# Kernel tuning notes

Measured on AMD Instinct MI355X. Metric: run time of the kernel, lower is better.

## Reference

```python
import jax, jax.numpy as jnp
import numpy as np

N = 4096          # number_of_node
DIN = 3           # dim_input (forced: fc1 expects N*dim_input == N*3 after last stage)
DOUT = 4          # dim_output
DACT = N          # dim_action defaults to number_of_node
B = 128


def setup_inputs() -> dict:
    key = jax.random.key(0)
    ks = jax.random.split(key, 12)
    X = jax.random.normal(ks[0], (B, N * DIN), dtype=jnp.float32)
    adj = jax.random.uniform(ks[1], (N, N), dtype=jnp.float32)
    def lin(kw, kb, fan_in, fan_out):
        bound = 1.0 / np.sqrt(fan_in)
        W = jax.random.uniform(kw, (fan_in, fan_out), minval=-bound, maxval=bound, dtype=jnp.float32)
        b = jax.random.uniform(kb, (fan_out,), minval=-bound, maxval=bound, dtype=jnp.float32)
        return W, b
    W1, b1 = lin(ks[2], ks[3], DIN, 4)
    W2, b2 = lin(ks[4], ks[5], 4, DOUT)
    W3, b3 = lin(ks[6], ks[7], DOUT, 3)
    Wfc, bfc = lin(ks[8], ks[9], N * DIN, 54)
    Wout, bout = lin(ks[10], ks[11], 54, DACT)
    return {"X": X, "adj": adj, "W1": W1, "b1": b1, "W2": W2, "b2": b2,
            "W3": W3, "b3": b3, "Wfc": Wfc, "bfc": bfc, "Wout": Wout, "bout": bout}


def reference(X, adj, W1, b1, W2, b2, W3, b3, Wfc, bfc, Wout, bout):
    # X: [B, N*DIN] -> [B, N, DIN]
    h = X.reshape(X.shape[0], N, DIN)
    # three (adj @ h) aggregations fused with tiny Linear + ReLU
    h = jax.nn.relu(jnp.einsum('nm,bmf->bnf', adj, h) @ W1 + b1)   # [B,N,4]
    h = jax.nn.relu(jnp.einsum('nm,bmf->bnf', adj, h) @ W2 + b2)   # [B,N,DOUT]
    h = jax.nn.relu(jnp.einsum('nm,bmf->bnf', adj, h) @ W3 + b3)   # [B,N,3]
    flat = h.reshape(h.shape[0], -1)                               # [B, N*3]
    hid = jax.nn.relu(flat @ Wfc + bfc)                            # [B, 54]
    q_value = hid @ Wout + bout                                    # [B, DACT]
    return q_value
```

## Files before the change

### kernel.cpp

```cpp
#include <hip/hip_runtime.h>


typedef __bf16 bf16x8 __attribute__((ext_vector_type(8)));
typedef float  f32x4  __attribute__((ext_vector_type(4)));

#define N_NODE 4096
#define BATCH  128

__device__ __forceinline__ void async_copy16(const void* gsrc, void* ldst) {
    __builtin_amdgcn_global_load_lds(
        (const __attribute__((address_space(1))) void*)gsrc,
        (__attribute__((address_space(3))) void*)ldst,
        16, 0, 0);
}

__global__ __launch_bounds__(256) void prep_k(const float* __restrict__ adj,
                                              __bf16* __restrict__ adjB,
                                              const float* __restrict__ X,
                                              const float* __restrict__ W1,
                                              __bf16* __restrict__ G0,
                                              float* __restrict__ hid_acc) {
    const int blk = blockIdx.x, tx = threadIdx.x;
    if (blk < 8192) {
        const size_t i = (size_t)blk * 256 + tx;
        const float4* a4 = (const float4*)adj;
        float4 u = a4[i * 2];
        float4 v = a4[i * 2 + 1];
        bf16x8 o = { (__bf16)u.x, (__bf16)u.y, (__bf16)u.z, (__bf16)u.w,
                     (__bf16)v.x, (__bf16)v.y, (__bf16)v.z, (__bf16)v.w };
        *(bf16x8*)(adjB + i * 8) = o;
    } else if (blk < 9216) {
        const int g = (blk - 8192) * 256 + tx;
        const int lp = g & 63, cbg = (g >> 6) & 31, kc = g >> 11;
        const int c = cbg * 16 + (lp & 15);
        const int b = c >> 2, f = c & 3;
        const float w0 = W1[0 * 4 + f], w1 = W1[1 * 4 + f], w2 = W1[2 * 4 + f];
        const int mb = kc * 32 + ((lp >> 4) & 3) * 8;
        const float* Xb = X + (size_t)b * 12288 + (size_t)mb * 3;
        bf16x8 o;
#pragma unroll
        for (int j = 0; j < 8; ++j) {
            const float v = Xb[j * 3 + 0] * w0 + Xb[j * 3 + 1] * w1 + Xb[j * 3 + 2] * w2;
            o[j] = (__bf16)v;
        }
        *(bf16x8*)(G0 + (size_t)g * 8) = o;
    } else {
        const int i = (blk - 9216) * 256 + tx;
        if (i < BATCH * 54) hid_acc[i] = 0.f;
    }
}

template <int MODE>
__global__ __launch_bounds__(256, 2) void gcn_k(const __bf16* __restrict__ A,
                                                const __bf16* __restrict__ Bp,
                                                const float* __restrict__ Wa,
                                                const float* __restrict__ ba,
                                                const float* __restrict__ Wb,
                                                __bf16* __restrict__ Op,
                                                float* __restrict__ H3out) {
    __shared__ __align__(16) unsigned char smem[65536];
    const int tx = threadIdx.x;
    const int wk = tx >> 6, lane = tx & 63;
    const int quad = lane >> 4, lr = lane & 15;

    const int l = blockIdx.x;
    const int xcd = l & 7, s = l >> 3;
    const int mi = xcd * 8 + (s & 7), ci = s >> 3;
    const int m0 = mi * 64, c0 = ci * 64;

    const __bf16* gA[4];
#pragma unroll
    for (int q = 0; q < 4; ++q) {
        const int c = q * 256 + tx;
        const int r = c >> 4, p = c & 15;
        const int lk = (p - r) & 15;
        gA[q] = A + (size_t)(m0 + r) * 4096 + lk * 8;
    }
    const __bf16* gB[4];
#pragma unroll
    for (int j = 0; j < 4; ++j)
        gB[j] = Bp + ((size_t)((wk * 32 + (ci * 4 + j)) * 64 + lane)) * 8;

    const int posw = ((wk * 4 + quad + lr) & 15) * 8;
    int foffA[4];
#pragma unroll
    for (int i = 0; i < 4; ++i) foffA[i] = (i * 16 + lr) * 128 + posw;

    f32x4 acc[4][4] = {};
    bf16x8 bv0[4], bv1[4], bv2[4], bv3[4];

#pragma unroll
    for (int q = 0; q < 4; ++q) async_copy16(gA[q], smem + q * 4096 + tx * 16);
#pragma unroll
    for (int j = 0; j < 4; ++j) bv0[j] = *(const bf16x8*)(gB[j]);
    asm volatile("" ::: "memory");
#pragma unroll
    for (int q = 0; q < 4; ++q) async_copy16(gA[q] + 128, smem + 16384 + q * 4096 + tx * 16);
#pragma unroll
    for (int j = 0; j < 4; ++j) bv1[j] = *(const bf16x8*)(gB[j] + 65536);
    asm volatile("" ::: "memory");
#pragma unroll
    for (int q = 0; q < 4; ++q) async_copy16(gA[q] + 256, smem + 32768 + q * 4096 + tx * 16);
#pragma unroll
    for (int j = 0; j < 4; ++j) bv2[j] = *(const bf16x8*)(gB[j] + 131072);
    asm volatile("" ::: "memory");

#define GCN_STEP(KT, P, WAIT, PF, CUR, NXT)                                    \
    {                                                                          \
        asm volatile(WAIT ::: "memory");                                       \
        __builtin_amdgcn_s_barrier();                                          \
        const __bf16* Ab = (const __bf16*)(smem + (P) * 16384);                \
        bf16x8 af[4];                                                          \
        _Pragma("unroll") for (int i = 0; i < 4; ++i)                          \
            af[i] = *(const bf16x8*)(Ab + foffA[i]);                           \
        if (PF) {                                                              \
            const int nt_ = (KT) + 3;                                          \
            unsigned char* bo_ = smem + (((P) + 3) & 3) * 16384;               \
            _Pragma("unroll") for (int q = 0; q < 4; ++q)                      \
                async_copy16(gA[q] + nt_ * 128, bo_ + q * 4096 + tx * 16);     \
            _Pragma("unroll") for (int j = 0; j < 4; ++j)                      \
                NXT[j] = *(const bf16x8*)(gB[j] + (size_t)nt_ * 65536);        \
        }                                                                      \
        __builtin_amdgcn_s_setprio(1);                                         \
        _Pragma("unroll") for (int i = 0; i < 4; ++i)                          \
            _Pragma("unroll") for (int j = 0; j < 4; ++j)                      \
                acc[i][j] = __builtin_amdgcn_mfma_f32_16x16x32_bf16(           \
                    af[i], CUR[j], acc[i][j], 0, 0, 0);                        \
        __builtin_amdgcn_s_setprio(0);                                         \
    }

    for (int kt = 0; kt < 28; kt += 4) {
        GCN_STEP(kt + 0, 0, "s_waitcnt vmcnt(16) lgkmcnt(0)", 1, bv0, bv3)
        GCN_STEP(kt + 1, 1, "s_waitcnt vmcnt(16) lgkmcnt(0)", 1, bv1, bv0)
        GCN_STEP(kt + 2, 2, "s_waitcnt vmcnt(16) lgkmcnt(0)", 1, bv2, bv1)
        GCN_STEP(kt + 3, 3, "s_waitcnt vmcnt(16) lgkmcnt(0)", 1, bv3, bv2)
    }
    GCN_STEP(28, 0, "s_waitcnt vmcnt(16) lgkmcnt(0)", 1, bv0, bv3)
    GCN_STEP(29, 1, "s_waitcnt vmcnt(16) lgkmcnt(0)", 0, bv1, bv0)
    GCN_STEP(30, 2, "s_waitcnt vmcnt(8) lgkmcnt(0)",  0, bv2, bv1)
    GCN_STEP(31, 3, "s_waitcnt vmcnt(0) lgkmcnt(0)",  0, bv3, bv2)
#undef GCN_STEP

    __syncthreads();
    float* part = (float*)smem;
    const int sb = (wk >> 1) * 4096;
    if (wk & 1) {
#pragma unroll
        for (int t = 0; t < 16; ++t)
            *(f32x4*)(part + sb + t * 256 + lane * 4) = acc[t >> 2][t & 3];
    }
    __syncthreads();
    if (!(wk & 1)) {
#pragma unroll
        for (int t = 0; t < 16; ++t)
            acc[t >> 2][t & 3] += *(const f32x4*)(part + sb + t * 256 + lane * 4);
    }
    __syncthreads();
    if (wk == 2) {
#pragma unroll
        for (int t = 0; t < 16; ++t)
            *(f32x4*)(part + t * 256 + lane * 4) = acc[t >> 2][t & 3];
    }
    __syncthreads();
    float* Ct = (float*)(smem + 32768);
    if (wk == 0) {
#pragma unroll
        for (int t = 0; t < 16; ++t)
            acc[t >> 2][t & 3] += *(const f32x4*)(part + t * 256 + lane * 4);
#pragma unroll
        for (int i = 0; i < 4; ++i)
#pragma unroll
            for (int j = 0; j < 4; ++j)
#pragma unroll
                for (int r = 0; r < 4; ++r)
                    Ct[(i * 16 + quad * 4 + r) * 66 + j * 16 + lr] = acc[i][j][r];
    }
    __syncthreads();

    if (MODE == 0) {
#pragma unroll
        for (int it = 0; it < 2; ++it) {
            const int g = it * 256 + tx;
            const int lp = g & 63, cbl = (g >> 6) & 3, kcl = g >> 8;
            const int cl = cbl * 16 + (lp & 15);
            const float bf = ba[cl & 3];
            const int mb = kcl * 32 + ((lp >> 4) & 3) * 8;
            bf16x8 o;
#pragma unroll
            for (int j = 0; j < 8; ++j)
                o[j] = (__bf16)fmaxf(Ct[(mb + j) * 66 + cl] + bf, 0.f);
            *(bf16x8*)(Op + ((size_t)((mi * 2 + kcl) * 32 + (ci * 4 + cbl)) * 64 + lp) * 8) = o;
        }
    } else if (MODE == 1) {
        float W2l[16], W3l[12], bl2[4];
#pragma unroll
        for (int i = 0; i < 16; ++i) W2l[i] = Wa[i];
#pragma unroll
        for (int i = 0; i < 12; ++i) W3l[i] = Wb[i];
#pragma unroll
        for (int i = 0; i < 4; ++i) bl2[i] = ba[i];
#pragma unroll
        for (int it = 0; it < 2; ++it) {
            const int g = it * 256 + tx;
            const int lp = g & 63, cbl = (g >> 6) & 3, kcl = g >> 8;
            const int cl = cbl * 16 + (lp & 15);
            const int bloc = cl >> 2, f3 = cl & 3;
            const int mb = kcl * 32 + ((lp >> 4) & 3) * 8;
            bf16x8 o;
#pragma unroll
            for (int j = 0; j < 8; ++j) {
                const float* row = &Ct[(mb + j) * 66 + bloc * 4];
                float v = 0.f;
                if (f3 < 3) {
#pragma unroll
                    for (int fo = 0; fo < 4; ++fo) {
                        const float tmp = fmaxf(row[0] * W2l[fo] + row[1] * W2l[4 + fo] +
                                                row[2] * W2l[8 + fo] + row[3] * W2l[12 + fo] +
                                                bl2[fo], 0.f);
                        const float w3a = W3l[fo * 3 + 0], w3b = W3l[fo * 3 + 1],
                                    w3c = W3l[fo * 3 + 2];
                        v += tmp * (f3 == 0 ? w3a : (f3 == 1 ? w3b : w3c));
                    }
                }
                o[j] = (__bf16)v;
            }
            *(bf16x8*)(Op + ((size_t)((mi * 2 + kcl) * 32 + (ci * 4 + cbl)) * 64 + lp) * 8) = o;
        }
    } else {
        const int m_l = tx & 63, cq = tx >> 6;
#pragma unroll
        for (int t = 0; t < 16; ++t) {
            const int cl = cq * 16 + t;
            const int c = c0 + cl, b = c >> 2, f = c & 3;
            if (f < 3)
                H3out[(size_t)(b * 3 + f) * N_NODE + m0 + m_l] =
                    fmaxf(Ct[m_l * 66 + cl] + ba[f], 0.f);
        }
    }
}

__global__ __launch_bounds__(256) void fc1p_k(const float* __restrict__ H3,
                                              const float* __restrict__ Wfc,
                                              float* __restrict__ hid_acc) {
    __shared__ float hs[16 * 192];
    __shared__ float red[4][16][64];
    const int tx = threadIdx.x;
    const int wv = tx >> 6, lane = tx & 63;
    const int n0 = blockIdx.x * 64;
    const int b0 = blockIdx.y * 16;

    for (int idx = tx; idx < 3072; idx += 256) {
        const int n = idx & 63, f = (idx >> 6) % 3, b = idx / 192;
        hs[idx] = H3[((size_t)((b0 + b) * 3 + f)) * N_NODE + n0 + n];
    }
    __syncthreads();

    float acc[16];
#pragma unroll
    for (int b = 0; b < 16; ++b) acc[b] = 0.f;
    if (lane < 54) {
        const int nb = wv * 16;
        for (int n = 0; n < 16; ++n) {
#pragma unroll
            for (int f = 0; f < 3; ++f) {
                const float w = Wfc[((size_t)(n0 + nb + n) * 3 + f) * 54 + lane];
#pragma unroll
                for (int b = 0; b < 16; ++b)
                    acc[b] += hs[b * 192 + f * 64 + nb + n] * w;
            }
        }
    }
#pragma unroll
    for (int b = 0; b < 16; ++b) red[wv][b][lane] = acc[b];
    __syncthreads();
    if (wv == 0 && lane < 54) {
        for (int b = 0; b < 16; ++b) {
            const float s = red[0][b][lane] + red[1][b][lane] +
                            red[2][b][lane] + red[3][b][lane];
            atomicAdd(&hid_acc[(b0 + b) * 54 + lane], s);
        }
    }
}

__global__ __launch_bounds__(256) void fc2_k(const float* __restrict__ hid_acc,
                                             const float* __restrict__ bfc,
                                             const float* __restrict__ Wout,
                                             const float* __restrict__ bout,
                                             float* __restrict__ out) {
    const int tx = threadIdx.x;
    const int a  = blockIdx.x * 256 + tx;
    const int b0 = blockIdx.y * 4;
    __shared__ float hs[4 * 54];
    if (tx < 216) {
        const int j = tx % 54;
        hs[tx] = fmaxf(hid_acc[b0 * 54 + tx] + bfc[j], 0.f);
    }
    __syncthreads();
    float a0 = 0.f, a1 = 0.f, a2 = 0.f, a3 = 0.f;
    for (int j = 0; j < 54; ++j) {
        float w = Wout[(size_t)j * N_NODE + a];
        a0 += hs[0 * 54 + j] * w;
        a1 += hs[1 * 54 + j] * w;
        a2 += hs[2 * 54 + j] * w;
        a3 += hs[3 * 54 + j] * w;
    }
    float bo = bout[a];
    out[(size_t)(b0 + 0) * N_NODE + a] = a0 + bo;
    out[(size_t)(b0 + 1) * N_NODE + a] = a1 + bo;
    out[(size_t)(b0 + 2) * N_NODE + a] = a2 + bo;
    out[(size_t)(b0 + 3) * N_NODE + a] = a3 + bo;
}

extern "C" void kernel_launch(void* const* d_in, const int* in_sizes, int n_in,
                              void* d_out, int out_size, void* d_ws, size_t ws_size,
                              hipStream_t stream) {
    const float* X    = (const float*)d_in[0];
    const float* adj  = (const float*)d_in[1];
    const float* W1   = (const float*)d_in[2];
    const float* b1   = (const float*)d_in[3];
    const float* W2   = (const float*)d_in[4];
    const float* b2   = (const float*)d_in[5];
    const float* W3   = (const float*)d_in[6];
    const float* b3   = (const float*)d_in[7];
    const float* Wfc  = (const float*)d_in[8];
    const float* bfc  = (const float*)d_in[9];
    const float* Wout = (const float*)d_in[10];
    const float* bout = (const float*)d_in[11];
    float* out = (float*)d_out;

    char* w = (char*)d_ws;
    __bf16* adjB = (__bf16*)w;
    __bf16* G0   = (__bf16*)(w + 33554432);
    __bf16* H1   = (__bf16*)(w + 33554432 + 4194304);
    __bf16* H2g  = (__bf16*)(w + 33554432 + 2 * 4194304);
    float*  H3   = (float*)(w + 33554432 + 3 * 4194304);
    float*  hid  = (float*)(w + 33554432 + 3 * 4194304 + 6291456);

    prep_k<<<9243, 256, 0, stream>>>(adj, adjB, X, W1, G0, hid);

    gcn_k<0><<<512, 256, 0, stream>>>(adjB, G0, nullptr, b1, nullptr, H1, nullptr);
    gcn_k<1><<<512, 256, 0, stream>>>(adjB, H1, W2, b2, W3, H2g, nullptr);
    gcn_k<2><<<512, 256, 0, stream>>>(adjB, H2g, nullptr, b3, nullptr, nullptr, H3);

    fc1p_k<<<dim3(64, 8), 256, 0, stream>>>(H3, Wfc, hid);
    fc2_k<<<dim3(16, 32), 256, 0, stream>>>(hid, bfc, Wout, bout, out);
}
```

Measured before the change: 225.2 us.

## Pre-swizzle adjacency into MFMA fragment layout and load A directly to registers

```diff
diff --git a/kernel.cpp b/kernel.cpp
--- a/kernel.cpp
+++ b/kernel.cpp
@@ -6,13 +6,6 @@
 
 #define N_NODE 4096
 #define BATCH  128
-
-__device__ __forceinline__ void async_copy16(const void* gsrc, void* ldst) {
-    __builtin_amdgcn_global_load_lds(
-        (const __attribute__((address_space(1))) void*)gsrc,
-        (__attribute__((address_space(3))) void*)ldst,
-        16, 0, 0);
-}
 
 __global__ __launch_bounds__(256) void prep_k(const float* __restrict__ adj,
                                               __bf16* __restrict__ adjB,
@@ -22,13 +15,16 @@
                                               float* __restrict__ hid_acc) {
     const int blk = blockIdx.x, tx = threadIdx.x;
     if (blk < 8192) {
-        const size_t i = (size_t)blk * 256 + tx;
-        const float4* a4 = (const float4*)adj;
-        float4 u = a4[i * 2];
-        float4 v = a4[i * 2 + 1];
+        const int g = blk * 256 + tx;
+        const int lane = g & 63, ka = (g >> 6) & 127, rb = g >> 13;
+        const int row = rb * 16 + (lane & 15);
+        const int kb  = ka * 32 + ((lane >> 4) & 3) * 8;
+        const float4* s = (const float4*)(adj + (size_t)row * 4096 + kb);
+        float4 u = s[0];
+        float4 v = s[1];
         bf16x8 o = { (__bf16)u.x, (__bf16)u.y, (__bf16)u.z, (__bf16)u.w,
                      (__bf16)v.x, (__bf16)v.y, (__bf16)v.z, (__bf16)v.w };
-        *(bf16x8*)(adjB + i * 8) = o;
+        *(bf16x8*)(adjB + (size_t)g * 8) = o;
     } else if (blk < 9216) {
         const int g = (blk - 8192) * 256 + tx;
         const int lp = g & 63, cbg = (g >> 6) & 31, kc = g >> 11;
@@ -58,7 +54,7 @@
                                                 const float* __restrict__ Wb,
                                                 __bf16* __restrict__ Op,
                                                 float* __restrict__ H3out) {
-    __shared__ __align__(16) unsigned char smem[65536];
+    __shared__ __align__(16) unsigned char smem[50688];
     const int tx = threadIdx.x;
     const int wk = tx >> 6, lane = tx & 63;
     const int quad = lane >> 4, lr = lane & 15;
@@ -68,78 +64,33 @@
     const int mi = xcd * 8 + (s & 7), ci = s >> 3;
     const int m0 = mi * 64, c0 = ci * 64;
 
-    const __bf16* gA[4];
-#pragma unroll
-    for (int q = 0; q < 4; ++q) {
-        const int c = q * 256 + tx;
-        const int r = c >> 4, p = c & 15;
-        const int lk = (p - r) & 15;
-        gA[q] = A + (size_t)(m0 + r) * 4096 + lk * 8;
-    }
-    const __bf16* gB[4];
+    const __bf16* pA[4];
+#pragma unroll
+    for (int i = 0; i < 4; ++i)
+        pA[i] = A + (size_t)(mi * 4 + i) * 65536 + wk * 512 + lane * 8;
+    const __bf16* pB[4];
 #pragma unroll
     for (int j = 0; j < 4; ++j)
-        gB[j] = Bp + ((size_t)((wk * 32 + (ci * 4 + j)) * 64 + lane)) * 8;
-
-    const int posw = ((wk * 4 + quad + lr) & 15) * 8;
-    int foffA[4];
-#pragma unroll
-    for (int i = 0; i < 4; ++i) foffA[i] = (i * 16 + lr) * 128 + posw;
+        pB[j] = Bp + (size_t)(wk * 32 + ci * 4 + j) * 512 + lane * 8;
 
     f32x4 acc[4][4] = {};
-    bf16x8 bv0[4], bv1[4], bv2[4], bv3[4];
-
-#pragma unroll
-    for (int q = 0; q < 4; ++q) async_copy16(gA[q], smem + q * 4096 + tx * 16);
-#pragma unroll
-    for (int j = 0; j < 4; ++j) bv0[j] = *(const bf16x8*)(gB[j]);
-    asm volatile("" ::: "memory");
-#pragma unroll
-    for (int q = 0; q < 4; ++q) async_copy16(gA[q] + 128, smem + 16384 + q * 4096 + tx * 16);
-#pragma unroll
-    for (int j = 0; j < 4; ++j) bv1[j] = *(const bf16x8*)(gB[j] + 65536);
-    asm volatile("" ::: "memory");
-#pragma unroll
-    for (int q = 0; q < 4; ++q) async_copy16(gA[q] + 256, smem + 32768 + q * 4096 + tx * 16);
-#pragma unroll
-    for (int j = 0; j < 4; ++j) bv2[j] = *(const bf16x8*)(gB[j] + 131072);
-    asm volatile("" ::: "memory");
-
-#define GCN_STEP(KT, P, WAIT, PF, CUR, NXT)                                    \
-    {                                                                          \
-        asm volatile(WAIT ::: "memory");                                       \
-        __builtin_amdgcn_s_barrier();                                          \
-        const __bf16* Ab = (const __bf16*)(smem + (P) * 16384);                \
-        bf16x8 af[4];                                                          \
-        _Pragma("unroll") for (int i = 0; i < 4; ++i)                          \
-            af[i] = *(const bf16x8*)(Ab + foffA[i]);                           \
-        if (PF) {                                                              \
-            const int nt_ = (KT) + 3;                                          \
-            unsigned char* bo_ = smem + (((P) + 3) & 3) * 16384;               \
-            _Pragma("unroll") for (int q = 0; q < 4; ++q)                      \
-                async_copy16(gA[q] + nt_ * 128, bo_ + q * 4096 + tx * 16);     \
-            _Pragma("unroll") for (int j = 0; j < 4; ++j)                      \
-                NXT[j] = *(const bf16x8*)(gB[j] + (size_t)nt_ * 65536);        \
-        }                                                                      \
-        __builtin_amdgcn_s_setprio(1);                                         \
-        _Pragma("unroll") for (int i = 0; i < 4; ++i)                          \
-            _Pragma("unroll") for (int j = 0; j < 4; ++j)                      \
-                acc[i][j] = __builtin_amdgcn_mfma_f32_16x16x32_bf16(           \
-                    af[i], CUR[j], acc[i][j], 0, 0, 0);                        \
-        __builtin_amdgcn_s_setprio(0);                                         \
-    }
-
-    for (int kt = 0; kt < 28; kt += 4) {
-        GCN_STEP(kt + 0, 0, "s_waitcnt vmcnt(16) lgkmcnt(0)", 1, bv0, bv3)
-        GCN_STEP(kt + 1, 1, "s_waitcnt vmcnt(16) lgkmcnt(0)", 1, bv1, bv0)
-        GCN_STEP(kt + 2, 2, "s_waitcnt vmcnt(16) lgkmcnt(0)", 1, bv2, bv1)
-        GCN_STEP(kt + 3, 3, "s_waitcnt vmcnt(16) lgkmcnt(0)", 1, bv3, bv2)
-    }
-    GCN_STEP(28, 0, "s_waitcnt vmcnt(16) lgkmcnt(0)", 1, bv0, bv3)
-    GCN_STEP(29, 1, "s_waitcnt vmcnt(16) lgkmcnt(0)", 0, bv1, bv0)
-    GCN_STEP(30, 2, "s_waitcnt vmcnt(8) lgkmcnt(0)",  0, bv2, bv1)
-    GCN_STEP(31, 3, "s_waitcnt vmcnt(0) lgkmcnt(0)",  0, bv3, bv2)
-#undef GCN_STEP
+
+#pragma unroll 4
+    for (int kt = 0; kt < 32; ++kt) {
+        bf16x8 af[4], bv[4];
+#pragma unroll
+        for (int i = 0; i < 4; ++i)
+            af[i] = *(const bf16x8*)(pA[i] + kt * 2048);
+#pragma unroll
+        for (int j = 0; j < 4; ++j)
+            bv[j] = *(const bf16x8*)(pB[j] + kt * 65536);
+#pragma unroll
+        for (int i = 0; i < 4; ++i)
+#pragma unroll
+            for (int j = 0; j < 4; ++j)
+                acc[i][j] = __builtin_amdgcn_mfma_f32_16x16x32_bf16(
+                    af[i], bv[j], acc[i][j], 0, 0, 0);
+    }
 
     __syncthreads();
     float* part = (float*)smem;
```

Measured after the change: 228.3 us. Within noise of the previous version (+1.4%).
